# Kernel tuning notes

Measured on AMD Instinct MI355X. Metric: run time of the kernel, lower is better.

Reference implementation:

```python
import jax, jax.numpy as jnp
import numpy as np

N_TAPS = 16
BATCH = 64
T = 480000  # 10 s @ 48 kHz, divisible by hop_length=256


def setup_inputs() -> dict:
    key = jax.random.key(0)
    k1, k2 = jax.random.split(key)
    x = jax.random.normal(k1, (BATCH, T), dtype=jnp.float32)
    b = jax.random.normal(k2, (N_TAPS,), dtype=jnp.float32) * 0.1
    return {"x": x, "b": b}


def reference(x, b):
    """Causal FIR filter: y[t] = sum_k b[k] * x[t-k], zero initial state.

    Equivalent to the torch module's per-timestep shift-register loop,
    expressed as one batched 1-D cross-correlation.
    """
    n = b.shape[0]
    # left-pad with n-1 zeros == zero-initialized shift register
    xp = jnp.pad(x, ((0, 0), (n - 1, 0)))[:, None, :]  # [B, 1, T+n-1]
    # lax.conv is cross-correlation; flip taps so w matches y[t]=sum b[k] x[t-k]
    w = b[::-1][None, None, :]  # [out=1, in=1, width=n]
    y = jax.lax.conv_general_dilated(
        xp, w, window_strides=(1,), padding='VALID',
        dimension_numbers=('NCH', 'OIH', 'NCH'))
    return y[:, 0, :]  # [B, T]
```

## Files before the change

### kernel.cpp

```cpp
#include <hip/hip_runtime.h>

#define BATCH 64
#define T 480000
#define T4 (T / 4)
#define NTAPS 16
#define TILE 512
#define SEGS 9
#define LDSC 576
#define TPR ((T4 + TILE - 1) / TILE)

typedef float floatx4 __attribute__((ext_vector_type(4)));

__global__ __launch_bounds__(256) void fir_tile_kernel(
    const float* __restrict__ x,
    const float* __restrict__ b,
    float* __restrict__ y)
{
    __shared__ floatx4 lds4[LDSC];

    const int tid  = threadIdx.x;
    const int lane = tid & 63;
    const int wave = tid >> 6;

    const int bid = blockIdx.x;
    const int r   = bid / TPR;
    const int t   = bid - r * TPR;

    const int    base_c = t * TILE - 4;
    const float* xrow   = x + (size_t)r * T;

    for (int seg = wave; seg < SEGS; seg += 4) {
        int c = base_c + seg * 64 + lane;
        c = c < 0 ? 0 : c;
        c = c > T4 - 1 ? T4 - 1 : c;
        const float* gp = xrow + (size_t)c * 4;
        __builtin_amdgcn_global_load_lds(
            (const __attribute__((address_space(1))) void*)gp,
            (__attribute__((address_space(3))) void*)((char*)&lds4[0] + seg * 1024),
            16, 0, 0);
    }

    float tap[NTAPS];
#pragma unroll
    for (int k = 0; k < NTAPS; ++k) tap[k] = b[k];

    __syncthreads();

    if (t == 0) {
        if (tid < 4) lds4[tid] = (floatx4){0.f, 0.f, 0.f, 0.f};
        __syncthreads();
    }

    floatx4* yv = (floatx4*)y + (size_t)r * T4;

#pragma unroll
    for (int p = 0; p < 2; ++p) {
        const int j  = tid + 256 * p;
        const int jo = j + 4;

        float s[20];
#pragma unroll
        for (int m = 0; m < 5; ++m) {
            floatx4 v = lds4[jo - 4 + m];
            s[4 * m + 0] = v.x;
            s[4 * m + 1] = v.y;
            s[4 * m + 2] = v.z;
            s[4 * m + 3] = v.w;
        }

        floatx4 out;
#pragma unroll
        for (int q = 0; q < 4; ++q) {
            float a = 0.f;
#pragma unroll
            for (int k = 0; k < NTAPS; ++k) a += tap[k] * s[16 + q - k];
            out[q] = a;
        }

        const int oc = t * TILE + j;
        if (oc < T4) yv[oc] = out;
    }
}

extern "C" void kernel_launch(void* const* d_in, const int* in_sizes, int n_in,
                              void* d_out, int out_size, void* d_ws, size_t ws_size,
                              hipStream_t stream)
{
    const float* x = (const float*)d_in[0];
    const float* b = (const float*)d_in[1];
    float* y = (float*)d_out;

    fir_tile_kernel<<<BATCH * TPR, 256, 0, stream>>>(x, b, y);
}
```

Baseline: 212.5 us.

## Convert FIR kernel to persistent grid with double-buffered LDS prefetch

```diff
diff --git a/kernel.cpp b/kernel.cpp
--- a/kernel.cpp
+++ b/kernel.cpp
@@ -5,67 +5,72 @@
 #define T4 (T / 4)
 #define NTAPS 16
 #define TILE 512
-#define SEGS 9
+#define TPR ((T4 + TILE - 1) / TILE)
+#define NTILES (BATCH * TPR)
 #define LDSC 576
-#define TPR ((T4 + TILE - 1) / TILE)
+#define GRID 2048
 
 typedef float floatx4 __attribute__((ext_vector_type(4)));
 
-__global__ __launch_bounds__(256) void fir_tile_kernel(
-    const float* __restrict__ x,
-    const float* __restrict__ b,
-    float* __restrict__ y)
+__device__ __forceinline__ void stage_tile(const float* __restrict__ x,
+                                           int g, floatx4* ldsbuf,
+                                           int lane, int wave)
 {
-    __shared__ floatx4 lds4[LDSC];
+    const int r      = g / TPR;
+    const int t      = g - r * TPR;
+    const int base_c = t * TILE - 4;
+    const float* xrow = x + (size_t)r * T;
 
-    const int tid  = threadIdx.x;
-    const int lane = tid & 63;
-    const int wave = tid >> 6;
-
-    const int bid = blockIdx.x;
-    const int r   = bid / TPR;
-    const int t   = bid - r * TPR;
-
-    const int    base_c = t * TILE - 4;
-    const float* xrow   = x + (size_t)r * T;
-
-    for (int seg = wave; seg < SEGS; seg += 4) {
+#pragma unroll
+    for (int s = 0; s < 2; ++s) {
+        const int seg = wave + 4 * s;
         int c = base_c + seg * 64 + lane;
         c = c < 0 ? 0 : c;
         c = c > T4 - 1 ? T4 - 1 : c;
         const float* gp = xrow + (size_t)c * 4;
         __builtin_amdgcn_global_load_lds(
             (const __attribute__((address_space(1))) void*)gp,
-            (__attribute__((address_space(3))) void*)((char*)&lds4[0] + seg * 1024),
+            (__attribute__((address_space(3))) void*)((char*)ldsbuf + seg * 1024),
             16, 0, 0);
     }
+    if (wave == 0 && lane < 4) {
+        int c = base_c + 512 + lane;
+        c = c < 0 ? 0 : c;
+        c = c > T4 - 1 ? T4 - 1 : c;
+        const float* gp = xrow + (size_t)c * 4;
+        __builtin_amdgcn_global_load_lds(
+            (const __attribute__((address_space(1))) void*)gp,
+            (__attribute__((address_space(3))) void*)((char*)ldsbuf + 512 * 16),
+            16, 0, 0);
+    }
+}
 
-    float tap[NTAPS];
-#pragma unroll
-    for (int k = 0; k < NTAPS; ++k) tap[k] = b[k];
-
-    __syncthreads();
-
-    if (t == 0) {
-        if (tid < 4) lds4[tid] = (floatx4){0.f, 0.f, 0.f, 0.f};
-        __syncthreads();
-    }
-
-    floatx4* yv = (floatx4*)y + (size_t)r * T4;
+__device__ __forceinline__ void compute_tile(int g, const floatx4* __restrict__ ldsbuf,
+                                             const float* __restrict__ tap,
+                                             floatx4* __restrict__ y4, int tid)
+{
+    const int r = g / TPR;
+    const int t = g - r * TPR;
+    floatx4* yv = y4 + (size_t)r * T4;
 
 #pragma unroll
     for (int p = 0; p < 2; ++p) {
-        const int j  = tid + 256 * p;
-        const int jo = j + 4;
+        const int j = tid + 256 * p;
 
         float s[20];
 #pragma unroll
         for (int m = 0; m < 5; ++m) {
-            floatx4 v = lds4[jo - 4 + m];
+            floatx4 v = ldsbuf[j + m];
             s[4 * m + 0] = v.x;
             s[4 * m + 1] = v.y;
             s[4 * m + 2] = v.z;
             s[4 * m + 3] = v.w;
+        }
+
+        if (t == 0) {
+#pragma unroll
+            for (int m = 0; m < 5; ++m)
+                if (j + m < 4) { s[4*m] = 0.f; s[4*m+1] = 0.f; s[4*m+2] = 0.f; s[4*m+3] = 0.f; }
         }
 
         floatx4 out;
@@ -82,6 +87,44 @@
     }
 }
 
+__global__ __launch_bounds__(256) void fir_pipe_kernel(
+    const float* __restrict__ x,
+    const float* __restrict__ b,
+    float* __restrict__ y)
+{
+    __shared__ floatx4 lds4[2][LDSC];
+
+    const int tid  = threadIdx.x;
+    const int lane = tid & 63;
+    const int wave = tid >> 6;
+
+    float tap[NTAPS];
+#pragma unroll
+    for (int k = 0; k < NTAPS; ++k) tap[k] = b[k];
+
+    floatx4* y4 = (floatx4*)y;
+
+    int g = blockIdx.x;
+    stage_tile(x, g, lds4[0], lane, wave);
+    asm volatile("s_waitcnt vmcnt(0)" ::: "memory");
+
+    int cur = 0;
+    for (; g < NTILES; g += GRID) {
+        const int gn = g + GRID;
+        if (gn < NTILES) {
+            stage_tile(x, gn, lds4[cur ^ 1], lane, wave);
+            if (wave == 0) asm volatile("s_waitcnt vmcnt(3)" ::: "memory");
+            else           asm volatile("s_waitcnt vmcnt(2)" ::: "memory");
+        } else {
+            asm volatile("s_waitcnt vmcnt(0)" ::: "memory");
+        }
+        __builtin_amdgcn_s_barrier();
+        compute_tile(g, lds4[cur], tap, y4, tid);
+        __builtin_amdgcn_s_barrier();
+        cur ^= 1;
+    }
+}
+
 extern "C" void kernel_launch(void* const* d_in, const int* in_sizes, int n_in,
                               void* d_out, int out_size, void* d_ws, size_t ws_size,
                               hipStream_t stream)
@@ -90,5 +133,5 @@
     const float* b = (const float*)d_in[1];
     float* y = (float*)d_out;
 
-    fir_tile_kernel<<<BATCH * TPR, 256, 0, stream>>>(x, b, y);
+    fir_pipe_kernel<<<GRID, 256, 0, stream>>>(x, b, y);
 }
```

Result: no change. 215.8 us (+1.5%).
